# Optimization experiments

Hardware: AMD Instinct MI355X
Metric: run time of the kernel (lower is better)

## Reference

```python
import jax, jax.numpy as jnp
import numpy as np

IGNORE = 255
KA = 10.0
ITERS = 10
BETA = 0.8


def _l2(x, axis):
    # F.normalize(p=2): divide by max(norm, eps)
    return x / jnp.maximum(jnp.linalg.norm(x, axis=axis, keepdims=True), 1e-12)


def setup_inputs() -> dict:
    key = jax.random.key(0)
    k1, k2, k3, k4 = jax.random.split(key, 4)
    B, K, P, C = 8, 19, 16384, 256
    return {
        "logit": jax.random.normal(k1, (B, K, P), jnp.float32),
        "target": jax.random.randint(k2, (B, P), 0, K, jnp.int32),
        "feat": jax.random.normal(k3, (B, C, P), jnp.float32),
        "epoch": 60,
        "prototypes_dataset": _l2(jax.random.normal(k4, (C, K), jnp.float32), 0),
    }


def reference(logit, target, feat, epoch, prototypes_dataset):
    B, K, P = logit.shape
    C = feat.shape[1]
    dt = feat.dtype

    # scatter-sum per-class prototypes over all (b, p) positions; ignore bucket = K
    index = jnp.where(target == IGNORE, K, target).reshape(-1)            # [B*P]
    feat_flat = jnp.swapaxes(feat, 1, 2).reshape(B * P, C)                # [B*P, C]
    proto = jax.ops.segment_sum(feat_flat, index, num_segments=K + 1)    # [K+1, C]
    counts = jax.ops.segment_sum(jnp.ones_like(index), index, num_segments=K + 1)
    prototypes_sum = proto[:K].T                                          # [C, K]
    counts_batch = counts[:K]                                             # [K]

    # epoch is a static python int; epoch >= start_epoch(51) -> full vMF branch
    feat_norm = _l2(feat, 1)                                              # [B, C, P]
    u_init = _l2(prototypes_sum / (counts_batch.astype(dt) + 1e-6), 0)    # [C, K]
    mask0 = counts_batch == 0
    u = _l2(jnp.where(mask0[None, :], prototypes_dataset, u_init), 0)     # 'part' init
    a = jnp.full((1, 1, K), 1.0 / K, dt)

    dis = jnp.einsum('bcp,ck->bpk', feat_norm, u)                         # [B, P, K]
    e = a * jnp.exp(KA * dis)
    p = e / jnp.sum(e, -1, keepdims=True)
    for _ in range(ITERS):
        # 'avmf': second assignment in torch overwrites -> mean over batch, [1, P, K]
        a = jnp.mean(p, 0, keepdims=True)
        # 'uvmf': new prototypes from soft assignments
        u = _l2(jnp.mean(jnp.einsum('bcp,bpk->bck', feat_norm, p), 0), 0)
        dis = jnp.einsum('bcp,ck->bpk', feat_norm, u)
        e = a * jnp.exp(KA * dis)
        p = e / jnp.sum(e, -1, keepdims=True)

    # vMF_hard_loss computed in torch but 'hard' not in loss_type -> not added
    vmf_loss = jnp.mean(-p * (jnp.log(a + 1e-6) + KA * dis)) / float(np.log(K))
    consist_loss = jnp.mean(-jnp.swapaxes(p, 1, 2) * jax.nn.log_softmax(logit, axis=1))

    # contrast: off-diagonal prototype similarity over classes present in batch
    m = (~mask0).astype(dt)
    gram = u_init.T @ u_init                                              # [K, K]
    Kn = jnp.sum(m)
    contrast_loss = (jnp.sum(gram * (m[:, None] * m[None, :])) - Kn) / (Kn * (Kn - 1))

    # 'tce': truncated CE, clamp per-pixel loss at -log(beta)
    logp = jax.nn.log_softmax(logit, axis=1)                              # [B, K, P]
    safe_t = jnp.where(target == IGNORE, 0, target)
    ce = -jnp.take_along_axis(logp, safe_t[:, None, :], axis=1)[:, 0, :]  # [B, P]
    valid = (target != IGNORE).astype(dt)
    loss = jnp.sum(jnp.maximum(ce, -float(np.log(BETA))) * valid) / (jnp.sum(valid) + 1e-6)

    loss = loss + vmf_loss + contrast_loss + consist_loss
    return (loss, jax.lax.stop_gradient(prototypes_sum), jax.lax.stop_gradient(counts_batch))
```

## Files before the change

kernel.cpp:

```cpp
#include <hip/hip_runtime.h>
#include <hip/hip_bf16.h>
#include <math.h>

#define BB 8
#define KK 19
#define PP 16384
#define CC 256
#define NN (BB*PP)
#define KA_C 10.0f
#define IGNORE_L 255
#define CETHR 0.22314355131420976f

#define OFF_FEATN   0
#define OFF_FEATNT  16777216
#define OFF_PROTO   33554432
#define OFF_COUNTS  (OFF_PROTO+4864)
#define OFF_SCAL    (OFF_COUNTS+32)
#define OFF_UINIT   (OFF_SCAL+16)
#define OFF_U       (OFF_UINIT+4864)
#define OFF_A       (OFF_U+4864)
#define OFF_UPART   (OFF_A+1245184)
#define OFF_R1      (OFF_UPART+2490368)
#define OFF_NORM    37343536

typedef __attribute__((ext_vector_type(8))) short short8v;
typedef __attribute__((ext_vector_type(4))) float f32x4;

static __device__ __forceinline__ float bflo(unsigned int v){
    union{unsigned int i; float f;} x; x.i = v << 16; return x.f;
}
static __device__ __forceinline__ unsigned short f2bf(float f){
    union{float f; unsigned int i;} x; x.f = f;
    unsigned int r = (x.i + 0x7fffu + ((x.i >> 16) & 1u)) >> 16;
    return (unsigned short)r;
}
static __device__ __forceinline__ float rowsum16(float v){
    v += __shfl_xor(v,1); v += __shfl_xor(v,2);
    v += __shfl_xor(v,4); v += __shfl_xor(v,8);
    return v;
}

__global__ __launch_bounds__(256) void counts_kernel(const int* __restrict__ target,
                                                     float* __restrict__ ws) {
    __shared__ int cnt[KK];
    if (threadIdx.x < KK) cnt[threadIdx.x]=0;
    __syncthreads();
    for (int i = blockIdx.x*256 + threadIdx.x; i < NN; i += gridDim.x*256) {
        int t = target[i];
        if (t >= 0 && t < KK) atomicAdd(&cnt[t], 1);
    }
    __syncthreads();
    if (threadIdx.x < KK) atomicAdd(&ws[OFF_COUNTS + threadIdx.x], (float)cnt[threadIdx.x]);
}

__global__ __launch_bounds__(256) void ssconv_kernel(const float* __restrict__ feat,
                                                     unsigned short* __restrict__ featn,
                                                     float* __restrict__ normf) {
    __shared__ float part[4][256];
    __shared__ float rn_lds[256];
    int blk = blockIdx.x;
    int b = blk >> 6;
    int px0 = (blk & 63) * 256;
    int tid = threadIdx.x;
    int lane = tid & 63, w = tid >> 6;
    int pxl = px0 + lane*4;
    const float* fb = feat + (size_t)b*CC*PP;
    int c0 = w*64;
    float a0=0.f,a1=0.f,a2=0.f,a3=0.f;
    for (int cc=0; cc<64; cc+=8) {
        float4 v[8];
#pragma unroll
        for (int j=0;j<8;j++) v[j] = *(const float4*)&fb[(size_t)(c0+cc+j)*PP + pxl];
#pragma unroll
        for (int j=0;j<8;j++) {
            a0=fmaf(v[j].x,v[j].x,a0); a1=fmaf(v[j].y,v[j].y,a1);
            a2=fmaf(v[j].z,v[j].z,a2); a3=fmaf(v[j].w,v[j].w,a3);
        }
    }
    *(float4*)&part[w][lane*4] = (float4){a0,a1,a2,a3};
    __syncthreads();
    float ss = part[0][tid]+part[1][tid]+part[2][tid]+part[3][tid];
    float nrm = fmaxf(sqrtf(ss), 1e-12f);
    normf[(size_t)b*PP + px0 + tid] = nrm;
    rn_lds[tid] = 1.0f/nrm;
    __syncthreads();
    float4 rv = *(const float4*)&rn_lds[lane*4];
    unsigned short* ob = featn + (size_t)b*CC*PP;
    for (int cc=0; cc<64; cc+=4) {
#pragma unroll
        for (int j=0;j<4;j++) {
            int c = c0+cc+j;
            float4 v = *(const float4*)&fb[(size_t)c*PP + pxl];
            ushort4 o;
            o.x=f2bf(v.x*rv.x); o.y=f2bf(v.y*rv.y);
            o.z=f2bf(v.z*rv.z); o.w=f2bf(v.w*rv.w);
            *(ushort4*)&ob[(size_t)c*PP + pxl] = o;
        }
    }
}

__global__ __launch_bounds__(256) void proto_mfma_kernel(const unsigned short* __restrict__ featn,
                                                         const int* __restrict__ target,
                                                         const float* __restrict__ normf,
                                                         float* __restrict__ upart) {
    __shared__ int tgt_lds[4][64];
    __shared__ unsigned short nrm_lds[4][64];
    int tid = threadIdx.x;
    int blk = blockIdx.x;
    int pxtile = blk & 255;
    int bgrp = blk >> 8;
    {
        int bi = tid >> 6, j = tid & 63;
        int bb = bgrp*4 + bi;
        tgt_lds[bi][j] = target[(size_t)bb*PP + pxtile*64 + j];
        nrm_lds[bi][j] = f2bf(normf[(size_t)bb*PP + pxtile*64 + j]);
    }
    __syncthreads();
    int lane = tid & 63, wid = tid >> 6;
    int g = lane >> 4, lc = lane & 15;

    f32x4 upacc[4][2];
#pragma unroll
    for (int m=0;m<4;m++)
#pragma unroll
        for (int n=0;n<2;n++) upacc[m][n] = (f32x4){0.f,0.f,0.f,0.f};

    for (int bi=0; bi<4; bi++) {
        int bb = bgrp*4 + bi;
        union { unsigned int u[4]; short8v s; } bfr[2][2];
#pragma unroll
        for (int ks=0; ks<2; ks++) {
            int pxo = ks*32 + g*8;
#pragma unroll
            for (int j2=0;j2<4;j2++) {
                int p0i = pxo + 2*j2, p1i = pxo + 2*j2 + 1;
                int t0 = tgt_lds[bi][p0i], t1 = tgt_lds[bi][p1i];
                unsigned int n0 = nrm_lds[bi][p0i], n1 = nrm_lds[bi][p1i];
                int kk1 = lc + 16;
                bfr[ks][0].u[j2] = (t0==lc ? n0:0u) | ((t1==lc ? n1:0u)<<16);
                bfr[ks][1].u[j2] = (t0==kk1? n0:0u) | ((t1==kk1? n1:0u)<<16);
            }
        }
#pragma unroll
        for (int m=0;m<4;m++) {
            int c = wid*64 + m*16 + lc;
            const unsigned short* fr = featn + ((size_t)bb*CC + c)*PP + pxtile*64;
#pragma unroll
            for (int ks=0; ks<2; ks++) {
                int pxo = ks*32 + g*8;
                union { uint4 u4; short8v s; } af2;
                af2.u4 = *(const uint4*)&fr[pxo];
                upacc[m][0] = __builtin_amdgcn_mfma_f32_16x16x32_bf16(af2.s, bfr[ks][0].s, upacc[m][0], 0,0,0);
                upacc[m][1] = __builtin_amdgcn_mfma_f32_16x16x32_bf16(af2.s, bfr[ks][1].s, upacc[m][1], 0,0,0);
            }
        }
    }
#pragma unroll
    for (int m=0;m<4;m++) {
        int cb = wid*64 + m*16 + g*4;
#pragma unroll
        for (int n=0;n<2;n++) {
            int kk = lc + 16*n;
            if (kk < KK) {
#pragma unroll
                for (int r=0;r<4;r++)
                    upart[(size_t)blk*4864 + (size_t)(cb+r)*KK + kk] = upacc[m][n][r];
            }
        }
    }
}

__global__ __launch_bounds__(256) void trans_kernel(const unsigned short* __restrict__ featn,
                                                    unsigned short* __restrict__ featn_T) {
    __shared__ unsigned short t_lds[64][260];
    int blk = blockIdx.x;
    int b = blk >> 8;
    int px0 = (blk & 255) * 64;
    int tid = threadIdx.x;
    const unsigned short* src = featn + ((size_t)b*CC + tid)*PP + px0;
#pragma unroll
    for (int j4=0; j4<8; j4++) {
        uint4 q = *(const uint4*)&src[j4*8];
        unsigned int w[4] = {q.x, q.y, q.z, q.w};
#pragma unroll
        for (int h=0;h<4;h++) {
            t_lds[j4*8 + 2*h    ][tid] = (unsigned short)(w[h] & 0xffffu);
            t_lds[j4*8 + 2*h + 1][tid] = (unsigned short)(w[h] >> 16);
        }
    }
    __syncthreads();
    unsigned short* dst = featn_T + ((size_t)b*PP + px0)*CC;
    for (int i = tid; i < 64*128; i += 256) {
        int row = i >> 7, c2 = (i & 127) * 2;
        unsigned int v = (unsigned int)t_lds[row][c2] | ((unsigned int)t_lds[row][c2+1] << 16);
        *(unsigned int*)&dst[(size_t)row*CC + c2] = v;
    }
}

__global__ __launch_bounds__(256) void setup_kernel(const float* __restrict__ pd,
                                                    float* __restrict__ ws) {
    int c = threadIdx.x;
    __shared__ float red[256];
    __shared__ float nrm[KK];
    __shared__ float lds_ui[256][KK];
    float cnts[KK], vi[KK];
#pragma unroll
    for (int k=0;k<KK;k++) cnts[k] = ws[OFF_COUNTS+k];
#pragma unroll
    for (int k=0;k<KK;k++) vi[k] = ws[OFF_PROTO + c*KK + k] / (cnts[k] + 1e-6f);
    for (int k=0;k<KK;k++) {
        red[c] = vi[k]*vi[k];
        __syncthreads();
        for (int s=128;s>0;s>>=1){ if (c<s) red[c]+=red[c+s]; __syncthreads(); }
        if (c==0) nrm[k] = fmaxf(sqrtf(red[0]), 1e-12f);
        __syncthreads();
    }
#pragma unroll
    for (int k=0;k<KK;k++) { vi[k] = vi[k]/nrm[k]; lds_ui[c][k] = vi[k]; ws[OFF_UINIT + c*KK + k] = vi[k]; }
    __syncthreads();
    float w0[KK];
#pragma unroll
    for (int k=0;k<KK;k++) w0[k] = (cnts[k]==0.f) ? pd[c*KK+k] : vi[k];
    for (int k=0;k<KK;k++) {
        red[c] = w0[k]*w0[k];
        __syncthreads();
        for (int s=128;s>0;s>>=1){ if (c<s) red[c]+=red[c+s]; __syncthreads(); }
        if (c==0) nrm[k] = fmaxf(sqrtf(red[0]), 1e-12f);
        __syncthreads();
    }
#pragma unroll
    for (int k=0;k<KK;k++) ws[OFF_U + k*CC + c] = w0[k] / nrm[k];
    float m[KK]; float Kn=0.f;
#pragma unroll
    for (int k=0;k<KK;k++){ m[k] = (cnts[k]==0.f)?0.f:1.f; Kn += m[k]; }
    float csum = 0.f;
    for (int idx = c; idx < KK*KK; idx += 256) {
        int k1 = idx / KK, k2 = idx % KK;
        if (m[k1]!=0.f && m[k2]!=0.f) {
            float gg=0.f;
            for (int cc2=0; cc2<CC; cc2++) gg += lds_ui[cc2][k1]*lds_ui[cc2][k2];
            csum += gg;
        }
    }
    red[c]=csum; __syncthreads();
    for (int s=128;s>0;s>>=1){ if (c<s) red[c]+=red[c+s]; __syncthreads(); }
    if (c==0) ws[OFF_SCAL+4] = (red[0] - Kn) / (Kn * (Kn - 1.f));
}

__global__ __launch_bounds__(256) void pu_kernel(const unsigned short* __restrict__ featn,
                                                 const unsigned short* __restrict__ featn_T,
                                                 const float* __restrict__ ubuf,
                                                 const float* __restrict__ aR0,
                                                 const float* __restrict__ aR1,
                                                 float* __restrict__ aW0,
                                                 float* __restrict__ aW1,
                                                 float* __restrict__ upart,
                                                 int uniform_a) {
    __shared__ __attribute__((aligned(16))) unsigned short u_lds[32*264];
    __shared__ __attribute__((aligned(16))) unsigned short p_lds[32*72];
    int tid = threadIdx.x;
    for (int i=tid; i<32*256; i+=256) {
        int k = i>>8, c = i&255;
        u_lds[k*264+c] = (k<KK) ? f2bf(ubuf[k*CC+c]) : (unsigned short)0;
    }
    __syncthreads();
    int blk = blockIdx.x;
    int pxtile = blk & 255;
    int bgrp = blk >> 8;
    int lane = tid & 63, wid = tid >> 6;
    int g = lane >> 4, lc = lane & 15;
    int px_w = pxtile*64 + wid*16;

    f32x4 upacc[4][2];
#pragma unroll
    for (int m=0;m<4;m++)
#pragma unroll
        for (int n=0;n<2;n++) upacc[m][n] = (f32x4){0.f,0.f,0.f,0.f};
    float aacc[2][4];
#pragma unroll
    for (int n=0;n<2;n++)
#pragma unroll
        for (int r=0;r<4;r++) aacc[n][r]=0.f;

    for (int bi=0; bi<4; bi++) {
        int bb = bgrp*4 + bi;
        const unsigned short* fb = featn + (size_t)bb*CC*PP;
        const unsigned short* fTrow = featn_T + ((size_t)bb*PP + px_w + lc)*CC;
        f32x4 acc0 = (f32x4){0.f,0.f,0.f,0.f};
        f32x4 acc1 = (f32x4){0.f,0.f,0.f,0.f};
#pragma unroll
        for (int ks=0; ks<8; ks++) {
            int cbase = ks*32 + g*8;
            union { uint4 u4; short8v s; } af, bf0, bf1;
            af.u4  = *(const uint4*)&fTrow[cbase];
            bf0.u4 = *(const uint4*)&u_lds[(size_t)lc*264 + cbase];
            bf1.u4 = *(const uint4*)&u_lds[(size_t)(lc+16)*264 + cbase];
            acc0 = __builtin_amdgcn_mfma_f32_16x16x32_bf16(af.s, bf0.s, acc0, 0,0,0);
            acc1 = __builtin_amdgcn_mfma_f32_16x16x32_bf16(af.s, bf1.s, acc1, 0,0,0);
        }
#pragma unroll
        for (int r=0;r<4;r++) {
            int pxg = px_w + g*4 + r;
            float a0, a1;
            if (uniform_a) { a0 = 1.0f/(float)KK; a1 = a0; }
            else {
                int k1 = (lc+16 > KK-1) ? (KK-1) : (lc+16);
                a0 = (aR0[(size_t)lc*PP+pxg] + aR1[(size_t)lc*PP+pxg])*0.125f;
                a1 = (aR0[(size_t)k1*PP+pxg] + aR1[(size_t)k1*PP+pxg])*0.125f;
            }
            float e0 = a0 * __expf(KA_C * acc0[r]);
            float e1 = (lc+16 < KK) ? a1 * __expf(KA_C * acc1[r]) : 0.f;
            float sv = rowsum16(e0 + e1);
            float inv = 1.0f/sv;
            float p0 = e0*inv, p1 = e1*inv;
            aacc[0][r] += p0; aacc[1][r] += p1;
            int pl = wid*16 + g*4 + r;
            p_lds[(size_t)lc*72 + pl]      = f2bf(p0);
            p_lds[(size_t)(lc+16)*72 + pl] = f2bf(p1);
        }
        __syncthreads();
#pragma unroll
        for (int m=0;m<4;m++) {
            int c = wid*64 + m*16 + lc;
            const unsigned short* fr = fb + (size_t)c*PP + pxtile*64;
#pragma unroll
            for (int ks=0; ks<2; ks++) {
                int pxo = ks*32 + g*8;
                union { uint4 u4; short8v s; } af2, bp0, bp1;
                af2.u4 = *(const uint4*)&fr[pxo];
                bp0.u4 = *(const uint4*)&p_lds[(size_t)lc*72 + pxo];
                bp1.u4 = *(const uint4*)&p_lds[(size_t)(lc+16)*72 + pxo];
                upacc[m][0] = __builtin_amdgcn_mfma_f32_16x16x32_bf16(af2.s, bp0.s, upacc[m][0], 0,0,0);
                upacc[m][1] = __builtin_amdgcn_mfma_f32_16x16x32_bf16(af2.s, bp1.s, upacc[m][1], 0,0,0);
            }
        }
        __syncthreads();
    }
#pragma unroll
    for (int m=0;m<4;m++) {
        int cb = wid*64 + m*16 + g*4;
#pragma unroll
        for (int n=0;n<2;n++) {
            int kk = lc + 16*n;
            if (kk < KK) {
#pragma unroll
                for (int r=0;r<4;r++)
                    upart[(size_t)blk*4864 + (size_t)(cb+r)*KK + kk] = upacc[m][n][r];
            }
        }
    }
    float* aOut = (bgrp==0) ? aW0 : aW1;
#pragma unroll
    for (int n=0;n<2;n++) {
        int kk = lc + 16*n;
        if (kk < KK) {
#pragma unroll
            for (int r=0;r<4;r++) {
                int pxg = px_w + g*4 + r;
                aOut[(size_t)kk*PP + pxg] = aacc[n][r];
            }
        }
    }
}

__global__ __launch_bounds__(256) void r1_kernel(const float* __restrict__ upart,
                                                 float* __restrict__ r1buf) {
    int blk = blockIdx.x;
    int echunk = blk % 19;
    int ichunk = blk / 19;
    int e = echunk*256 + threadIdx.x;
    float s = 0.f;
    int i0 = ichunk*64;
    for (int i=i0; i<i0+64; i++) s += upart[(size_t)i*4864 + e];
    r1buf[(size_t)ichunk*4864 + e] = s;
}

__global__ __launch_bounds__(256) void r2_kernel(const float* __restrict__ r1buf,
                                                 float* __restrict__ ws) {
    int k = blockIdx.x;
    int c = threadIdx.x;
    float s = 0.f;
#pragma unroll
    for (int i=0;i<8;i++) s += r1buf[(size_t)i*4864 + c*KK + k];
    __shared__ float red[256];
    red[c] = s*s; __syncthreads();
    for (int q=128;q>0;q>>=1){ if (c<q) red[c]+=red[c+q]; __syncthreads(); }
    float nrm = fmaxf(sqrtf(red[0]), 1e-12f);
    ws[OFF_U + k*CC + c] = s / nrm;
}

__global__ __launch_bounds__(256) void protored2_kernel(const float* __restrict__ r1buf,
                                                        float* __restrict__ ws) {
    int e = blockIdx.x*256 + threadIdx.x;
    float s = 0.f;
#pragma unroll
    for (int i=0;i<8;i++) s += r1buf[(size_t)i*4864 + e];
    ws[OFF_PROTO + e] = s;
}

__global__ __launch_bounds__(256) void final_kernel(const unsigned short* __restrict__ featn,
                                                    const float* __restrict__ logit,
                                                    const int* __restrict__ target,
                                                    const float* __restrict__ ws_u,
                                                    const float* __restrict__ aF0,
                                                    const float* __restrict__ aF1,
                                                    float* __restrict__ scal) {
    __shared__ float lu[4864];
    for (int i=threadIdx.x; i<4864; i+=256) lu[i] = ws_u[i];
    __syncthreads();
    int n = blockIdx.x*256 + threadIdx.x;
    int b = n >> 14;
    int pix = n & (PP-1);
    const unsigned short* fcol = featn + (size_t)b*CC*PP + pix;
    float dot[KK];
#pragma unroll
    for (int k=0;k<KK;k++) dot[k]=0.f;
    for (int c0=0; c0<CC; c0+=16) {
        float fv[16];
#pragma unroll
        for (int j=0;j<16;j++) {
            unsigned int u16 = fcol[(size_t)(c0+j)*PP];
            fv[j] = bflo(u16);
        }
#pragma unroll
        for (int k=0;k<KK;k++) {
            float d = dot[k];
#pragma unroll
            for (int j=0;j<16;j++) d = fmaf(fv[j], lu[k*CC+c0+j], d);
            dot[k]=d;
        }
    }
    float e[KK]; float den=0.f;
#pragma unroll
    for (int k=0;k<KK;k++) {
        float av = (aF0[(size_t)k*PP + pix] + aF1[(size_t)k*PP + pix])*0.125f;
        e[k] = av * __expf(KA_C * dot[k]);
        den += e[k];
    }
    float inv = 1.0f/den;
    float vmf = 0.f;
#pragma unroll
    for (int k=0;k<KK;k++) {
        float av = (aF0[(size_t)k*PP + pix] + aF1[(size_t)k*PP + pix])*0.125f;
        vmf += -(e[k]*inv) * (__logf(av + 1e-6f) + KA_C * dot[k]);
    }
    float lg[KK]; float mx = -3.4e38f;
#pragma unroll
    for (int k=0;k<KK;k++) { lg[k] = logit[((size_t)b*KK + k)*PP + pix]; mx = fmaxf(mx, lg[k]); }
    float sme = 0.f;
#pragma unroll
    for (int k=0;k<KK;k++) sme += __expf(lg[k]-mx);
    float lse = mx + __logf(sme);
    float cons = 0.f;
#pragma unroll
    for (int k=0;k<KK;k++) cons += -(e[k]*inv) * (lg[k]-lse);
    int t = target[(size_t)b*PP + pix];
    float ce_n = 0.f, ce_d = 0.f;
    if (t != IGNORE_L) {
        float lt = 0.f;
#pragma unroll
        for (int k=0;k<KK;k++) lt = (t==k) ? lg[k] : lt;
        float ce = -(lt - lse);
        ce_n = fmaxf(ce, CETHR);
        ce_d = 1.f;
    }
    __shared__ float red[4][4];
    int lane = threadIdx.x & 63, w = threadIdx.x >> 6;
    float v0=vmf, v1=cons, v2=ce_n, v3=ce_d;
#pragma unroll
    for (int s=32;s>0;s>>=1) {
        v0 += __shfl_xor(v0, s); v1 += __shfl_xor(v1, s);
        v2 += __shfl_xor(v2, s); v3 += __shfl_xor(v3, s);
    }
    if (lane==0){ red[w][0]=v0; red[w][1]=v1; red[w][2]=v2; red[w][3]=v3; }
    __syncthreads();
    if (threadIdx.x==0) {
        atomicAdd(&scal[0], red[0][0]+red[1][0]+red[2][0]+red[3][0]);
        atomicAdd(&scal[1], red[0][1]+red[1][1]+red[2][1]+red[3][1]);
        atomicAdd(&scal[2], red[0][2]+red[1][2]+red[2][2]+red[3][2]);
        atomicAdd(&scal[3], red[0][3]+red[1][3]+red[2][3]+red[3][3]);
    }
}

__global__ __launch_bounds__(256) void finalize_kernel(const float* __restrict__ ws,
                                                       float* __restrict__ out) {
    if (blockIdx.x==0 && threadIdx.x==0) {
        float cnt_all = (float)BB*(float)PP*(float)KK;
        float vmf  = ws[OFF_SCAL+0] / cnt_all / logf((float)KK);
        float cons = ws[OFF_SCAL+1] / cnt_all;
        float ce   = ws[OFF_SCAL+2] / (ws[OFF_SCAL+3] + 1e-6f);
        float contrast = ws[OFF_SCAL+4];
        out[0] = ce + vmf + contrast + cons;
    }
    int i = blockIdx.x*256 + threadIdx.x;
    if (i < 4864) out[1+i] = ws[OFF_PROTO+i];
    if (blockIdx.x==0 && threadIdx.x < KK) out[1+4864+threadIdx.x] = ws[OFF_COUNTS+threadIdx.x];
}

extern "C" void kernel_launch(void* const* d_in, const int* in_sizes, int n_in,
                              void* d_out, int out_size, void* d_ws, size_t ws_size,
                              hipStream_t stream) {
    (void)in_sizes; (void)n_in; (void)out_size; (void)ws_size;
    const float* logit  = (const float*)d_in[0];
    const int*   target = (const int*)d_in[1];
    const float* feat   = (const float*)d_in[2];
    const float* pd     = (const float*)d_in[4];
    float* out = (float*)d_out;
    float* ws  = (float*)d_ws;

    unsigned short* featn   = (unsigned short*)ws;
    unsigned short* featn_T = (unsigned short*)(ws + OFF_FEATNT);
    float* ubuf  = ws + OFF_U;
    float* upart = ws + OFF_UPART;
    float* r1buf = ws + OFF_R1;
    float* normf = ws + OFF_NORM;
    float* scal  = ws + OFF_SCAL;
    float* aH[4];
    for (int q=0;q<4;q++) aH[q] = ws + OFF_A + (size_t)q*311296;

    hipMemsetAsync(ws + OFF_PROTO, 0, 4912*sizeof(float), stream);
    ssconv_kernel<<<512, 256, 0, stream>>>(feat, featn, normf);
    counts_kernel<<<256, 256, 0, stream>>>(target, ws);
    proto_mfma_kernel<<<512, 256, 0, stream>>>(featn, target, normf, upart);
    r1_kernel<<<152, 256, 0, stream>>>(upart, r1buf);
    protored2_kernel<<<19, 256, 0, stream>>>(r1buf, ws);
    setup_kernel<<<1, 256, 0, stream>>>(pd, ws);
    trans_kernel<<<BB*256, 256, 0, stream>>>(featn, featn_T);

    pu_kernel<<<512, 256, 0, stream>>>(featn, featn_T, ubuf,
                                       aH[0], aH[1], aH[2], aH[3], upart, 1);
    for (int t=1; t<10; t++) {
        int ri = (t&1)*2;
        int wi = ((t+1)&1)*2;
        r1_kernel<<<152, 256, 0, stream>>>(upart, r1buf);
        r2_kernel<<<KK, 256, 0, stream>>>(r1buf, ws);
        pu_kernel<<<512, 256, 0, stream>>>(featn, featn_T, ubuf,
                                           aH[ri], aH[ri+1], aH[wi], aH[wi+1],
                                           upart, 0);
    }
    r1_kernel<<<152, 256, 0, stream>>>(upart, r1buf);
    r2_kernel<<<KK, 256, 0, stream>>>(r1buf, ws);
    final_kernel<<<512, 256, 0, stream>>>(featn, logit, target, ubuf, aH[0], aH[1], scal);
    finalize_kernel<<<20, 256, 0, stream>>>(ws, out);
}
```

Measured before the change: 693.5 us.

## Fuse transpose into normalize kernel and split pu_kernel batch groups across more blocks

Merges the separate transpose pass into the normalization kernel, so the transposed bf16 copy is written straight from registers through LDS and the normalized buffer is no longer re-read. pu_kernel now processes 2 batches per block instead of 4, doubling the grid to 1024 blocks. The soft-assignment partials become four buffers per set, summed on read, and the prior loads are hoisted out of the batch loop. Reductions now cover 16 partial buffers, which adds workspace and reduction traffic in exchange for more parallelism in the iterative kernel.

Result: faster. 673.0 us (-3.0%).

```diff
diff --git a/kernel.cpp b/kernel.cpp
--- a/kernel.cpp
+++ b/kernel.cpp
@@ -10,6 +10,7 @@
 #define KA_C 10.0f
 #define IGNORE_L 255
 #define CETHR 0.22314355131420976f
+#define ASTRIDE 311296
 
 #define OFF_FEATN   0
 #define OFF_FEATNT  16777216
@@ -19,9 +20,9 @@
 #define OFF_UINIT   (OFF_SCAL+16)
 #define OFF_U       (OFF_UINIT+4864)
 #define OFF_A       (OFF_U+4864)
-#define OFF_UPART   (OFF_A+1245184)
-#define OFF_R1      (OFF_UPART+2490368)
-#define OFF_NORM    37343536
+#define OFF_UPART   (OFF_A+2490368)
+#define OFF_R1      (OFF_UPART+4980736)
+#define OFF_NORM    (OFF_R1+77824)
 
 typedef __attribute__((ext_vector_type(8))) short short8v;
 typedef __attribute__((ext_vector_type(4))) float f32x4;
@@ -53,49 +54,64 @@
     if (threadIdx.x < KK) atomicAdd(&ws[OFF_COUNTS + threadIdx.x], (float)cnt[threadIdx.x]);
 }
 
-__global__ __launch_bounds__(256) void ssconv_kernel(const float* __restrict__ feat,
-                                                     unsigned short* __restrict__ featn,
-                                                     float* __restrict__ normf) {
-    __shared__ float part[4][256];
-    __shared__ float rn_lds[256];
+__global__ __launch_bounds__(256) void ssct_kernel(const float* __restrict__ feat,
+                                                   unsigned short* __restrict__ featn,
+                                                   unsigned short* __restrict__ featn_T,
+                                                   float* __restrict__ normf) {
+    __shared__ float part[4][128];
+    __shared__ float rn_lds[128];
+    __shared__ unsigned short tT[128][35];
     int blk = blockIdx.x;
-    int b = blk >> 6;
-    int px0 = (blk & 63) * 256;
+    int b = blk >> 7;
+    int px0 = (blk & 127) * 128;
     int tid = threadIdx.x;
     int lane = tid & 63, w = tid >> 6;
-    int pxl = px0 + lane*4;
+    int pxl = px0 + lane*2;
     const float* fb = feat + (size_t)b*CC*PP;
-    int c0 = w*64;
-    float a0=0.f,a1=0.f,a2=0.f,a3=0.f;
+    float a0=0.f, a1=0.f;
     for (int cc=0; cc<64; cc+=8) {
-        float4 v[8];
-#pragma unroll
-        for (int j=0;j<8;j++) v[j] = *(const float4*)&fb[(size_t)(c0+cc+j)*PP + pxl];
-#pragma unroll
-        for (int j=0;j<8;j++) {
-            a0=fmaf(v[j].x,v[j].x,a0); a1=fmaf(v[j].y,v[j].y,a1);
-            a2=fmaf(v[j].z,v[j].z,a2); a3=fmaf(v[j].w,v[j].w,a3);
-        }
-    }
-    *(float4*)&part[w][lane*4] = (float4){a0,a1,a2,a3};
-    __syncthreads();
-    float ss = part[0][tid]+part[1][tid]+part[2][tid]+part[3][tid];
-    float nrm = fmaxf(sqrtf(ss), 1e-12f);
-    normf[(size_t)b*PP + px0 + tid] = nrm;
-    rn_lds[tid] = 1.0f/nrm;
-    __syncthreads();
-    float4 rv = *(const float4*)&rn_lds[lane*4];
-    unsigned short* ob = featn + (size_t)b*CC*PP;
-    for (int cc=0; cc<64; cc+=4) {
-#pragma unroll
-        for (int j=0;j<4;j++) {
-            int c = c0+cc+j;
-            float4 v = *(const float4*)&fb[(size_t)c*PP + pxl];
-            ushort4 o;
-            o.x=f2bf(v.x*rv.x); o.y=f2bf(v.y*rv.y);
-            o.z=f2bf(v.z*rv.z); o.w=f2bf(v.w*rv.w);
-            *(ushort4*)&ob[(size_t)c*PP + pxl] = o;
-        }
+        float2 v[8];
+#pragma unroll
+        for (int j=0;j<8;j++) v[j] = *(const float2*)&fb[(size_t)(w*64+cc+j)*PP + pxl];
+#pragma unroll
+        for (int j=0;j<8;j++) { a0 = fmaf(v[j].x,v[j].x,a0); a1 = fmaf(v[j].y,v[j].y,a1); }
+    }
+    part[w][lane*2]   = a0;
+    part[w][lane*2+1] = a1;
+    __syncthreads();
+    if (tid < 128) {
+        float ss = part[0][tid]+part[1][tid]+part[2][tid]+part[3][tid];
+        float nrm = fmaxf(sqrtf(ss), 1e-12f);
+        normf[(size_t)b*PP + px0 + tid] = nrm;
+        rn_lds[tid] = 1.0f/nrm;
+    }
+    __syncthreads();
+    float rv0 = rn_lds[lane*2], rv1 = rn_lds[lane*2+1];
+    unsigned short* ob  = featn + (size_t)b*CC*PP;
+    unsigned short* obT = featn_T + ((size_t)b*PP + px0)*CC;
+    for (int sl=0; sl<8; sl++) {
+        int c0s = sl*32;
+#pragma unroll
+        for (int jj=0; jj<8; jj++) {
+            int cl = w*8 + jj;
+            int c = c0s + cl;
+            float2 v = *(const float2*)&fb[(size_t)c*PP + pxl];
+            unsigned int lo = f2bf(v.x*rv0);
+            unsigned int hi = f2bf(v.y*rv1);
+            *(unsigned int*)&ob[(size_t)c*PP + pxl] = (hi<<16)|lo;
+            tT[lane*2][cl]   = (unsigned short)lo;
+            tT[lane*2+1][cl] = (unsigned short)hi;
+        }
+        __syncthreads();
+#pragma unroll
+        for (int j=0; j<8; j++) {
+            int flat = j*256 + tid;
+            int px = flat >> 4;
+            int cu = flat & 15;
+            unsigned int v = (unsigned int)tT[px][cu*2] | ((unsigned int)tT[px][cu*2+1] << 16);
+            *(unsigned int*)&obT[(size_t)px*CC + c0s + cu*2] = v;
+        }
+        __syncthreads();
     }
 }
 
@@ -170,33 +186,6 @@
     }
 }
 
-__global__ __launch_bounds__(256) void trans_kernel(const unsigned short* __restrict__ featn,
-                                                    unsigned short* __restrict__ featn_T) {
-    __shared__ unsigned short t_lds[64][260];
-    int blk = blockIdx.x;
-    int b = blk >> 8;
-    int px0 = (blk & 255) * 64;
-    int tid = threadIdx.x;
-    const unsigned short* src = featn + ((size_t)b*CC + tid)*PP + px0;
-#pragma unroll
-    for (int j4=0; j4<8; j4++) {
-        uint4 q = *(const uint4*)&src[j4*8];
-        unsigned int w[4] = {q.x, q.y, q.z, q.w};
-#pragma unroll
-        for (int h=0;h<4;h++) {
-            t_lds[j4*8 + 2*h    ][tid] = (unsigned short)(w[h] & 0xffffu);
-            t_lds[j4*8 + 2*h + 1][tid] = (unsigned short)(w[h] >> 16);
-        }
-    }
-    __syncthreads();
-    unsigned short* dst = featn_T + ((size_t)b*PP + px0)*CC;
-    for (int i = tid; i < 64*128; i += 256) {
-        int row = i >> 7, c2 = (i & 127) * 2;
-        unsigned int v = (unsigned int)t_lds[row][c2] | ((unsigned int)t_lds[row][c2+1] << 16);
-        *(unsigned int*)&dst[(size_t)row*CC + c2] = v;
-    }
-}
-
 __global__ __launch_bounds__(256) void setup_kernel(const float* __restrict__ pd,
                                                     float* __restrict__ ws) {
     int c = threadIdx.x;
@@ -250,10 +239,8 @@
 __global__ __launch_bounds__(256) void pu_kernel(const unsigned short* __restrict__ featn,
                                                  const unsigned short* __restrict__ featn_T,
                                                  const float* __restrict__ ubuf,
-                                                 const float* __restrict__ aR0,
-                                                 const float* __restrict__ aR1,
-                                                 float* __restrict__ aW0,
-                                                 float* __restrict__ aW1,
+                                                 const float* __restrict__ aRbase,
+                                                 float* __restrict__ aWbase,
                                                  float* __restrict__ upart,
                                                  int uniform_a) {
     __shared__ __attribute__((aligned(16))) unsigned short u_lds[32*264];
@@ -271,6 +258,24 @@
     int g = lane >> 4, lc = lane & 15;
     int px_w = pxtile*64 + wid*16;
 
+    float a0r[4], a1r[4];
+    if (uniform_a) {
+#pragma unroll
+        for (int r=0;r<4;r++){ a0r[r]=1.0f/(float)KK; a1r[r]=1.0f/(float)KK; }
+    } else {
+        int k1 = (lc+16 > KK-1) ? (KK-1) : (lc+16);
+#pragma unroll
+        for (int r=0;r<4;r++) {
+            int pxg = px_w + g*4 + r;
+            float s0 = aRbase[0*ASTRIDE + (size_t)lc*PP+pxg] + aRbase[1*ASTRIDE + (size_t)lc*PP+pxg]
+                     + aRbase[2*ASTRIDE + (size_t)lc*PP+pxg] + aRbase[3*ASTRIDE + (size_t)lc*PP+pxg];
+            float s1 = aRbase[0*ASTRIDE + (size_t)k1*PP+pxg] + aRbase[1*ASTRIDE + (size_t)k1*PP+pxg]
+                     + aRbase[2*ASTRIDE + (size_t)k1*PP+pxg] + aRbase[3*ASTRIDE + (size_t)k1*PP+pxg];
+            a0r[r] = s0*0.125f;
+            a1r[r] = s1*0.125f;
+        }
+    }
+
     f32x4 upacc[4][2];
 #pragma unroll
     for (int m=0;m<4;m++)
@@ -282,8 +287,8 @@
 #pragma unroll
         for (int r=0;r<4;r++) aacc[n][r]=0.f;
 
-    for (int bi=0; bi<4; bi++) {
-        int bb = bgrp*4 + bi;
+    for (int bi=0; bi<2; bi++) {
+        int bb = bgrp*2 + bi;
         const unsigned short* fb = featn + (size_t)bb*CC*PP;
         const unsigned short* fTrow = featn_T + ((size_t)bb*PP + px_w + lc)*CC;
         f32x4 acc0 = (f32x4){0.f,0.f,0.f,0.f};
@@ -300,16 +305,8 @@
         }
 #pragma unroll
         for (int r=0;r<4;r++) {
-            int pxg = px_w + g*4 + r;
-            float a0, a1;
-            if (uniform_a) { a0 = 1.0f/(float)KK; a1 = a0; }
-            else {
-                int k1 = (lc+16 > KK-1) ? (KK-1) : (lc+16);
-                a0 = (aR0[(size_t)lc*PP+pxg] + aR1[(size_t)lc*PP+pxg])*0.125f;
-                a1 = (aR0[(size_t)k1*PP+pxg] + aR1[(size_t)k1*PP+pxg])*0.125f;
-            }
-            float e0 = a0 * __expf(KA_C * acc0[r]);
-            float e1 = (lc+16 < KK) ? a1 * __expf(KA_C * acc1[r]) : 0.f;
+            float e0 = a0r[r] * __expf(KA_C * acc0[r]);
+            float e1 = (lc+16 < KK) ? a1r[r] * __expf(KA_C * acc1[r]) : 0.f;
             float sv = rowsum16(e0 + e1);
             float inv = 1.0f/sv;
             float p0 = e0*inv, p1 = e1*inv;
@@ -349,7 +346,7 @@
             }
         }
     }
-    float* aOut = (bgrp==0) ? aW0 : aW1;
+    float* aOut = aWbase + (size_t)bgrp*ASTRIDE;
 #pragma unroll
     for (int n=0;n<2;n++) {
         int kk = lc + 16*n;
@@ -376,12 +373,11 @@
 }
 
 __global__ __launch_bounds__(256) void r2_kernel(const float* __restrict__ r1buf,
-                                                 float* __restrict__ ws) {
+                                                 float* __restrict__ ws, int nbuf) {
     int k = blockIdx.x;
     int c = threadIdx.x;
     float s = 0.f;
-#pragma unroll
-    for (int i=0;i<8;i++) s += r1buf[(size_t)i*4864 + c*KK + k];
+    for (int i=0;i<nbuf;i++) s += r1buf[(size_t)i*4864 + c*KK + k];
     __shared__ float red[256];
     red[c] = s*s; __syncthreads();
     for (int q=128;q>0;q>>=1){ if (c<q) red[c]+=red[c+q]; __syncthreads(); }
@@ -390,11 +386,10 @@
 }
 
 __global__ __launch_bounds__(256) void protored2_kernel(const float* __restrict__ r1buf,
-                                                        float* __restrict__ ws) {
+                                                        float* __restrict__ ws, int nbuf) {
     int e = blockIdx.x*256 + threadIdx.x;
     float s = 0.f;
-#pragma unroll
-    for (int i=0;i<8;i++) s += r1buf[(size_t)i*4864 + e];
+    for (int i=0;i<nbuf;i++) s += r1buf[(size_t)i*4864 + e];
     ws[OFF_PROTO + e] = s;
 }
 
@@ -402,8 +397,7 @@
                                                     const float* __restrict__ logit,
                                                     const int* __restrict__ target,
                                                     const float* __restrict__ ws_u,
-                                                    const float* __restrict__ aF0,
-                                                    const float* __restrict__ aF1,
+                                                    const float* __restrict__ aFbase,
                                                     float* __restrict__ scal) {
     __shared__ float lu[4864];
     for (int i=threadIdx.x; i<4864; i+=256) lu[i] = ws_u[i];
@@ -430,19 +424,19 @@
             dot[k]=d;
         }
     }
-    float e[KK]; float den=0.f;
+    float e[KK]; float den=0.f; float av[KK];
 #pragma unroll
     for (int k=0;k<KK;k++) {
-        float av = (aF0[(size_t)k*PP + pix] + aF1[(size_t)k*PP + pix])*0.125f;
-        e[k] = av * __expf(KA_C * dot[k]);
+        av[k] = (aFbase[0*ASTRIDE + (size_t)k*PP + pix] + aFbase[1*ASTRIDE + (size_t)k*PP + pix]
+               + aFbase[2*ASTRIDE + (size_t)k*PP + pix] + aFbase[3*ASTRIDE + (size_t)k*PP + pix])*0.125f;
+        e[k] = av[k] * __expf(KA_C * dot[k]);
         den += e[k];
     }
     float inv = 1.0f/den;
     float vmf = 0.f;
 #pragma unroll
     for (int k=0;k<KK;k++) {
-        float av = (aF0[(size_t)k*PP + pix] + aF1[(size_t)k*PP + pix])*0.125f;
-        vmf += -(e[k]*inv) * (__logf(av + 1e-6f) + KA_C * dot[k]);
+        vmf += -(e[k]*inv) * (__logf(av[k] + 1e-6f) + KA_C * dot[k]);
     }
     float lg[KK]; float mx = -3.4e38f;
 #pragma unroll
@@ -515,31 +509,27 @@
     float* r1buf = ws + OFF_R1;
     float* normf = ws + OFF_NORM;
     float* scal  = ws + OFF_SCAL;
-    float* aH[4];
-    for (int q=0;q<4;q++) aH[q] = ws + OFF_A + (size_t)q*311296;
+    float* aSet[2] = { ws + OFF_A, ws + OFF_A + (size_t)4*ASTRIDE };
 
     hipMemsetAsync(ws + OFF_PROTO, 0, 4912*sizeof(float), stream);
-    ssconv_kernel<<<512, 256, 0, stream>>>(feat, featn, normf);
+    ssct_kernel<<<1024, 256, 0, stream>>>(feat, featn, featn_T, normf);
     counts_kernel<<<256, 256, 0, stream>>>(target, ws);
     proto_mfma_kernel<<<512, 256, 0, stream>>>(featn, target, normf, upart);
     r1_kernel<<<152, 256, 0, stream>>>(upart, r1buf);
-    protored2_kernel<<<19, 256, 0, stream>>>(r1buf, ws);
+    protored2_kernel<<<19, 256, 0, stream>>>(r1buf, ws, 8);
     setup_kernel<<<1, 256, 0, stream>>>(pd, ws);
-    trans_kernel<<<BB*256, 256, 0, stream>>>(featn, featn_T);
-
-    pu_kernel<<<512, 256, 0, stream>>>(featn, featn_T, ubuf,
-                                       aH[0], aH[1], aH[2], aH[3], upart, 1);
-    for (int t=1; t<10; t++) {
-        int ri = (t&1)*2;
-        int wi = ((t+1)&1)*2;
-        r1_kernel<<<152, 256, 0, stream>>>(upart, r1buf);
-        r2_kernel<<<KK, 256, 0, stream>>>(r1buf, ws);
-        pu_kernel<<<512, 256, 0, stream>>>(featn, featn_T, ubuf,
-                                           aH[ri], aH[ri+1], aH[wi], aH[wi+1],
-                                           upart, 0);
-    }
-    r1_kernel<<<152, 256, 0, stream>>>(upart, r1buf);
-    r2_kernel<<<KK, 256, 0, stream>>>(r1buf, ws);
-    final_kernel<<<512, 256, 0, stream>>>(featn, logit, target, ubuf, aH[0], aH[1], scal);
+
+    for (int t=0; t<10; t++) {
+        if (t > 0) {
+            r1_kernel<<<304, 256, 0, stream>>>(upart, r1buf);
+            r2_kernel<<<KK, 256, 0, stream>>>(r1buf, ws, 16);
+        }
+        pu_kernel<<<1024, 256, 0, stream>>>(featn, featn_T, ubuf,
+                                            aSet[t&1], aSet[(t+1)&1],
+                                            upart, (t==0)?1:0);
+    }
+    r1_kernel<<<304, 256, 0, stream>>>(upart, r1buf);
+    r2_kernel<<<KK, 256, 0, stream>>>(r1buf, ws, 16);
+    final_kernel<<<512, 256, 0, stream>>>(featn, logit, target, ubuf, aSet[0], scal);
     finalize_kernel<<<20, 256, 0, stream>>>(ws, out);
 }
```
